# Optimization experiments

Measured on AMD Instinct MI355X. Metric: run time of the kernel, lower is better.

## Reference

```python
import jax, jax.numpy as jnp
import numpy as np

FEAT_STRIDE = 16
PRE_NMS_TOPN = 6000
POST_NMS_TOPN = 300
NMS_THRESH = 0.7
MIN_SIZE = 16.0
NEG = -1e9


def _whctrs(a):
    w = a[2] - a[0] + 1.0
    h = a[3] - a[1] + 1.0
    return w, h, a[0] + 0.5 * (w - 1), a[1] + 0.5 * (h - 1)


def _mkanchors(ws, hs, xc, yc):
    return np.stack([xc - 0.5 * (ws - 1), yc - 0.5 * (hs - 1),
                     xc + 0.5 * (ws - 1), yc + 0.5 * (hs - 1)], axis=1)


def generate_anchors(base_size=16, ratios=(0.5, 1.0, 2.0), scales=(8, 16, 32)):
    base = np.array([0, 0, base_size - 1, base_size - 1], dtype=np.float64)
    w, h, xc, yc = _whctrs(base)
    size = w * h
    ratios = np.array(ratios, dtype=np.float64)
    ws = np.round(np.sqrt(size / ratios))
    hs = np.round(ws * ratios)
    ratio_anchors = _mkanchors(ws, hs, xc, yc)
    out = []
    for a in ratio_anchors:
        w, h, xc, yc = _whctrs(a)
        s = np.array(scales, dtype=np.float64)
        out.append(_mkanchors(w * s, h * s, xc, yc))
    return np.concatenate(out, axis=0).astype(np.float32)


def _nms_single(boxes, scores):
    # boxes [N,4], scores [N] (sorted desc by top_k); greedy NMS, fixed POST_NMS_TOPN picks
    x1, y1, x2, y2 = boxes[:, 0], boxes[:, 1], boxes[:, 2], boxes[:, 3]
    areas = (x2 - x1 + 1.0) * (y2 - y1 + 1.0)

    def body(i, st):
        keep, ok, live = st
        s = jnp.where(live, scores, NEG - 1.0)
        j = jnp.argmax(s)
        valid = s[j] > NEG / 2
        keep = keep.at[i].set(j.astype(jnp.int32))
        ok = ok.at[i].set(valid)
        xx1 = jnp.maximum(x1[j], x1)
        yy1 = jnp.maximum(y1[j], y1)
        xx2 = jnp.minimum(x2[j], x2)
        yy2 = jnp.minimum(y2[j], y2)
        inter = jnp.maximum(xx2 - xx1 + 1.0, 0.0) * jnp.maximum(yy2 - yy1 + 1.0, 0.0)
        iou = inter / (areas[j] + areas - inter)
        live = live & (iou <= NMS_THRESH)
        return keep, ok, live

    keep0 = jnp.zeros((POST_NMS_TOPN,), jnp.int32)
    ok0 = jnp.zeros((POST_NMS_TOPN,), bool)
    live0 = scores > NEG / 2
    keep, ok, _ = jax.lax.fori_loop(0, POST_NMS_TOPN, body, (keep0, ok0, live0))
    return keep, ok


def _proposals(rpn_cls_prob, rpn_bbox_pred, im_info, anchors):
    B, _, H, W = rpn_cls_prob.shape
    A = anchors.shape[0]
    # fg scores: second half of the 2A channel dim
    scores = rpn_cls_prob[:, A:].transpose(0, 2, 3, 1).reshape(B, -1)          # [B, H*W*A]
    deltas = rpn_bbox_pred.transpose(0, 2, 3, 1).reshape(B, -1, 4)             # [B, H*W*A, 4]
    # shifted anchors over the feature map
    sx = (jnp.arange(W, dtype=jnp.float32)) * FEAT_STRIDE
    sy = (jnp.arange(H, dtype=jnp.float32)) * FEAT_STRIDE
    gx, gy = jnp.meshgrid(sx, sy)                                              # [H, W]
    shifts = jnp.stack([gx.ravel(), gy.ravel(), gx.ravel(), gy.ravel()], 1)    # [K, 4]
    all_anchors = (shifts[:, None, :] + anchors[None, :, :]).reshape(-1, 4)    # [K*A, 4]
    # bbox_transform_inv
    wa = all_anchors[:, 2] - all_anchors[:, 0] + 1.0
    ha = all_anchors[:, 3] - all_anchors[:, 1] + 1.0
    cxa = all_anchors[:, 0] + 0.5 * (wa - 1.0)
    cya = all_anchors[:, 1] + 0.5 * (ha - 1.0)
    dx, dy, dw, dh = deltas[..., 0], deltas[..., 1], deltas[..., 2], deltas[..., 3]
    cx = dx * wa + cxa
    cy = dy * ha + cya
    pw = jnp.exp(dw) * wa
    ph = jnp.exp(dh) * ha
    x1 = cx - 0.5 * (pw - 1.0)
    y1 = cy - 0.5 * (ph - 1.0)
    x2 = cx + 0.5 * (pw - 1.0)
    y2 = cy + 0.5 * (ph - 1.0)
    # clip to image
    imh = im_info[:, 0:1]
    imw = im_info[:, 1:2]
    x1 = jnp.clip(x1, 0.0, imw - 1.0)
    y1 = jnp.clip(y1, 0.0, imh - 1.0)
    x2 = jnp.clip(x2, 0.0, imw - 1.0)
    y2 = jnp.clip(y2, 0.0, imh - 1.0)
    boxes = jnp.stack([x1, y1, x2, y2], axis=-1)                               # [B, N, 4]
    # filter boxes smaller than min_size * im_scale (mask by score)
    min_sz = MIN_SIZE * im_info[:, 2:3]
    keep_m = ((x2 - x1 + 1.0) >= min_sz) & ((y2 - y1 + 1.0) >= min_sz)
    scores = jnp.where(keep_m, scores, NEG)
    # pre-NMS top-k
    scores_top, order = jax.lax.top_k(scores, PRE_NMS_TOPN)                    # [B, 6000]
    boxes_top = jnp.take_along_axis(boxes, order[:, :, None], axis=1)          # [B, 6000, 4]
    # greedy NMS per image
    keep, keep_ok = jax.vmap(_nms_single)(boxes_top, scores_top)               # [B, 300]
    sel = jnp.take_along_axis(boxes_top, keep[:, :, None], axis=1)             # [B, 300, 4]
    sel = jnp.where(keep_ok[:, :, None], sel, 0.0)
    bidx = jnp.broadcast_to(jnp.arange(B, dtype=sel.dtype)[:, None, None], (B, POST_NMS_TOPN, 1))
    return jnp.concatenate([bidx, sel], axis=-1)                               # [B, 300, 5]


def setup_inputs() -> dict:
    key = jax.random.key(0)
    k1, k2 = jax.random.split(key)
    B, H, W, A = 32, 100, 100, 9
    rpn_cls_prob = jax.random.uniform(k1, (B, 2 * A, H, W), dtype=jnp.float32)
    rpn_bbox_pred = jax.random.normal(k2, (B, 4 * A, H, W), dtype=jnp.float32) * 0.2
    im_info = jnp.tile(jnp.array([[1600.0, 1600.0, 1.0]], dtype=jnp.float32), (B, 1))
    anchors = jnp.asarray(generate_anchors(base_size=16, ratios=(0.5, 1.0, 2.0), scales=(8, 16, 32)))
    return {"rpn_cls_prob": rpn_cls_prob, "rpn_bbox_pred": rpn_bbox_pred,
            "im_info": im_info, "anchors": anchors}


def reference(rpn_cls_prob, rpn_bbox_pred, im_info, anchors):
    return _proposals(rpn_cls_prob, rpn_bbox_pred, im_info, anchors)
```

## Files before the change

kernel.cpp:

```cpp
#include <hip/hip_runtime.h>

#define NB 32
#define NA 9
#define FH 100
#define FW 100
#define HWSZ (FH*FW)
#define NANCH (HWSZ*NA)
#define PRE 6000
#define POST 300
#define SORTN 8192
#define NEGV -1000000000.0f
#define NMS_T 0.7f
#define MARG 1e-4f
#define NCHUNK ((PRE + 63) / 64)
#define WB() __builtin_amdgcn_wave_barrier()
#define NSLICE 11
#define DSLICE 8192

typedef unsigned long long u64;
typedef unsigned int u32;

__device__ __forceinline__ u32 f2sort(float f) {
  u32 u = __float_as_uint(f);
  return (u & 0x80000000u) ? ~u : (u | 0x80000000u);
}

__device__ __forceinline__ float4 decode_box(const float* __restrict__ pred,
                                             const float* __restrict__ anchors,
                                             int b, int i, float imw, float imh) {
  int hw = i / NA; int a = i - hw * NA;
  int h = hw / FW; int w = hw - h * FW;
  float sx = (float)(w * 16);
  float sy = (float)(h * 16);
  float ax1 = anchors[a*4+0] + sx, ay1 = anchors[a*4+1] + sy;
  float ax2 = anchors[a*4+2] + sx, ay2 = anchors[a*4+3] + sy;
  float wa = ax2 - ax1 + 1.0f, ha = ay2 - ay1 + 1.0f;
  float cxa = ax1 + 0.5f*(wa - 1.0f), cya = ay1 + 0.5f*(ha - 1.0f);
  size_t base = (((size_t)b*36 + a*4)*FH + h)*FW + w;
  float dx = pred[base];
  float dy = pred[base + HWSZ];
  float dw = pred[base + 2*HWSZ];
  float dh = pred[base + 3*HWSZ];
  float cx = dx*wa + cxa, cy = dy*ha + cya;
  float pw = expf(dw)*wa, ph = expf(dh)*ha;
  float x1 = fminf(fmaxf(cx - 0.5f*(pw - 1.0f), 0.0f), imw - 1.0f);
  float y1 = fminf(fmaxf(cy - 0.5f*(ph - 1.0f), 0.0f), imh - 1.0f);
  float x2 = fminf(fmaxf(cx + 0.5f*(pw - 1.0f), 0.0f), imw - 1.0f);
  float y2 = fminf(fmaxf(cy + 0.5f*(ph - 1.0f), 0.0f), imh - 1.0f);
  return make_float4(x1, y1, x2, y2);
}

__global__ void k_zero(u32* __restrict__ histcnt, u32* __restrict__ cand32) {
  int i = blockIdx.x * 1024 + threadIdx.x;
  if (i < 262144) histcnt[i] = 0;
  cand32[i] = 0;
}

__global__ __launch_bounds__(1024) void k_decode(
    const float* __restrict__ cls,
    const float* __restrict__ pred,
    const float* __restrict__ iminfo,
    const float* __restrict__ anchors,
    u32* __restrict__ scoreg,
    u32* __restrict__ histg) {
  __shared__ u32 hl[4096];
  const int blk = blockIdx.x;
  const int b = blk / NSLICE, s = blk - b * NSLICE;
  const int tid = threadIdx.x;
  for (int j = tid; j < 4096; j += 1024) hl[j] = 0;
  __syncthreads();
  const float imh = iminfo[b*3+0], imw = iminfo[b*3+1], sc = iminfo[b*3+2];
  const float msz = 16.0f * sc;
  #pragma unroll
  for (int r = 0; r < 8; ++r) {
    int i = s * DSLICE + r * 1024 + tid;
    if (i < NANCH) {
      int hw = i / NA; int a = i - hw * NA;
      int h = hw / FW; int w = hw - h * FW;
      float score = cls[(((size_t)b*18 + 9 + a)*FH + h)*FW + w];
      float4 bx = decode_box(pred, anchors, b, i, imw, imh);
      bool keep = ((bx.z - bx.x + 1.0f) >= msz) && ((bx.w - bx.y + 1.0f) >= msz);
      float sf = keep ? score : NEGV;
      float t = sf * 4096.0f;
      int bin = (t <= 0.0f) ? 0 : ((t >= 4095.0f) ? 4095 : (int)t);
      atomicAdd(&hl[bin], 1u);
      scoreg[(size_t)b * NANCH + i] = f2sort(sf);
    }
  }
  __syncthreads();
  for (int j = tid; j < 4096; j += 1024) {
    u32 v = hl[j];
    if (v) atomicAdd(&histg[b * 4096 + j], v);
  }
}

__device__ __forceinline__ void w0_cut(u32* hist, u32 target, int lane,
                                       int* cutBin) {
  u32 cs = 0;
  int cb = lane * 64;
  for (int i = 0; i < 64; ++i) cs += hist[cb + ((i + lane) & 63)];
  u32 suf = cs;
  #pragma unroll
  for (int d = 1; d < 64; d <<= 1) {
    u32 o = __shfl_down(suf, (unsigned)d, 64);
    suf += (lane < 64 - d) ? o : 0u;
  }
  u64 m1 = __ballot(suf >= target);
  int L = 63 - __clzll(m1);
  u32 nAb = (L < 63) ? (u32)__builtin_amdgcn_readlane((int)suf, L + 1) : 0u;
  u32 fs = hist[L * 64 + lane];
  #pragma unroll
  for (int d = 1; d < 64; d <<= 1) {
    u32 o = __shfl_down(fs, (unsigned)d, 64);
    fs += (lane < 64 - d) ? o : 0u;
  }
  fs += nAb;
  u64 m2 = __ballot(fs >= target);
  int fb = 63 - __clzll(m2);
  *cutBin = L * 64 + fb;
}

__global__ __launch_bounds__(64) void k_cut(const u32* __restrict__ histg,
                                            u32* __restrict__ thrTg,
                                            u32* __restrict__ binStartG) {
  __shared__ u32 hl[4096];
  const int b = blockIdx.x, lane = threadIdx.x;
  const u32* h = histg + b * 4096;
  for (int i = lane; i < 4096; i += 64) hl[i] = h[i];
  __syncthreads();
  int L;
  w0_cut(hl, PRE, lane, &L);
  u32 running = 0;
  for (int hi = 4095; hi >= L; hi -= 64) {
    int bin = hi - lane;
    u32 c = (bin >= L && bin >= 0) ? hl[bin] : 0u;
    u32 p = c;
    #pragma unroll
    for (int d = 1; d < 64; d <<= 1) {
      u32 o = __shfl_up(p, (unsigned)d, 64);
      if (lane >= d) p += o;
    }
    if (bin >= L && bin >= 0) binStartG[b * 4096 + bin] = running + p - c;
    running += (u32)__builtin_amdgcn_readlane((int)p, 63);
  }
  if (lane == 0) thrTg[b] = f2sort((float)L * (1.0f / 4096.0f));
}

__global__ __launch_bounds__(1024) void k_scatter(
    const u32* __restrict__ scoreg,
    const u32* __restrict__ thrTg,
    const u32* __restrict__ binStartG,
    u32* __restrict__ binCntG,
    u64* __restrict__ candg) {
  const int blk = blockIdx.x;
  const int b = blk / NSLICE, s = blk - b * NSLICE;
  const int tid = threadIdx.x;
  const u32 thrT = thrTg[b];
  const u32* sb = scoreg + (size_t)b * NANCH;
  #pragma unroll
  for (int r = 0; r < 8; ++r) {
    int i = s * DSLICE + r * 1024 + tid;
    if (i < NANCH) {
      u32 sv = sb[i];
      if (sv >= thrT) {
        float f = __uint_as_float(sv ^ 0x80000000u);
        float t = f * 4096.0f;
        int bin = (t >= 4095.0f) ? 4095 : (int)t;
        u32 pos = binStartG[b * 4096 + bin] + atomicAdd(&binCntG[b * 4096 + bin], 1u);
        if (pos < SORTN) candg[(size_t)b * SORTN + pos] = ((u64)sv << 32) | (u32)(~(u32)i);
      }
    }
  }
}

__global__ __launch_bounds__(1024) void k_binsort(
    const u32* __restrict__ binStartG,
    const u32* __restrict__ binCntG,
    u64* __restrict__ candg) {
  __shared__ u64 sc[16][512];
  const int wave = threadIdx.x >> 6, lane = threadIdx.x & 63;
  const int task = blockIdx.x * 16 + wave;
  const int b = task >> 12, bin = task & 4095;
  u32 cnt = binCntG[b * 4096 + bin];
  if (cnt < 2) return;
  u32 base = binStartG[b * 4096 + bin];
  if (base >= SORTN) return;
  u32 m = cnt;
  if (base + m > SORTN) m = SORTN - base;
  u64* seg = candg + (size_t)b * SORTN + base;
  if (m <= 64) {
    u64 v = (lane < (int)m) ? seg[lane] : 0ull;
    #pragma unroll
    for (int k = 2; k <= 64; k <<= 1) {
      for (int j = k >> 1; j > 0; j >>= 1) {
        u64 o = __shfl_xor((unsigned long long)v, j, 64);
        bool dirD = ((lane & k) == 0);
        bool lower = ((lane & j) == 0);
        bool takeMax = (dirD == lower);
        bool sw = takeMax ? (o > v) : (o < v);
        if (sw) v = o;
      }
    }
    if (lane < (int)m) seg[lane] = v;
  } else if (m <= 512) {
    int np = 128; while (np < (int)m) np <<= 1;
    for (int i = lane; i < np; i += 64) sc[wave][i] = (i < (int)m) ? seg[i] : 0ull;
    WB();
    for (int k = 2; k <= np; k <<= 1) {
      for (int j = k >> 1; j > 0; j >>= 1) {
        for (int q = lane; q < np/2; q += 64) {
          int i = ((q & ~(j-1)) << 1) | (q & (j-1));
          int x = i | j;
          u64 a0 = sc[wave][i], a1 = sc[wave][x];
          bool up = (i & k) != 0;
          if (up ? (a0 > a1) : (a0 < a1)) { sc[wave][i] = a1; sc[wave][x] = a0; }
        }
        WB();
      }
    }
    for (int i = lane; i < (int)m; i += 64) seg[i] = sc[wave][i];
  }
}

#define SMEM_BYTES 103424
__global__ __launch_bounds__(1024, 1) void k_nms(
    const u64* __restrict__ candg,
    const float* __restrict__ pred,
    const float* __restrict__ iminfo,
    const float* __restrict__ anchors,
    float* __restrict__ out) {
  __shared__ __align__(16) unsigned char smemRaw[SMEM_BYTES];
  float4* boxes = (float4*)smemRaw;
  u64* liveM = (u64*)(smemRaw + 96256);
  float4* accB = (float4*)(smemRaw + 97024);
  float* accA = (float*)(smemRaw + 101824);
  u64* okm = (u64*)(smemRaw + 103040);
  int* scal = (int*)(smemRaw + 103168);
  float* aL = (float*)(smemRaw + 103232);

  const int b = blockIdx.x;
  const int tid = threadIdx.x;
  const int wave = tid >> 6, lane = tid & 63;
  const u32 liveThr = f2sort(-5.0e8f);
  const u64* cb = candg + (size_t)b * SORTN;

  if (tid < 36) aL[tid] = anchors[tid];
  if (tid == 0) scal[4] = 0;
  __syncthreads();

  const float imh = iminfo[b*3+0], imw = iminfo[b*3+1];
  #pragma unroll
  for (int r = 0; r < 6; ++r) {
    int c = wave + 16 * r;
    if (c < NCHUNK) {
      int i = tid + 1024 * r;
      u64 k = cb[i];
      int idx = (int)(~(u32)k);
      bool v = (u32)idx < (u32)NANCH;
      bool live = ((u32)(k >> 32) > liveThr) && v && (i < PRE);
      int id = v ? idx : 0;
      int hw = id / NA; int a = id - hw * NA;
      int h = hw / FW; int w = hw - h * FW;
      float sx = (float)(w * 16), sy = (float)(h * 16);
      float ax1 = aL[a*4+0] + sx, ay1 = aL[a*4+1] + sy;
      float ax2 = aL[a*4+2] + sx, ay2 = aL[a*4+3] + sy;
      float wa = ax2 - ax1 + 1.0f, ha = ay2 - ay1 + 1.0f;
      float cxa = ax1 + 0.5f*(wa - 1.0f), cya = ay1 + 0.5f*(ha - 1.0f);
      size_t base = (((size_t)b*36 + a*4)*FH + h)*FW + w;
      float dx = pred[base], dy = pred[base + HWSZ];
      float dw = pred[base + 2*HWSZ], dh = pred[base + 3*HWSZ];
      float cx = dx*wa + cxa, cy = dy*ha + cya;
      float pw = expf(dw)*wa, ph = expf(dh)*ha;
      float4 bc;
      bc.x = fminf(fmaxf(cx - 0.5f*(pw - 1.0f), 0.0f), imw - 1.0f);
      bc.y = fminf(fmaxf(cy - 0.5f*(ph - 1.0f), 0.0f), imh - 1.0f);
      bc.z = fminf(fmaxf(cx + 0.5f*(pw - 1.0f), 0.0f), imw - 1.0f);
      bc.w = fminf(fmaxf(cy + 0.5f*(ph - 1.0f), 0.0f), imh - 1.0f);
      boxes[i] = bc;
      u64 lm = __ballot(live);
      if (lane == 0) liveM[c] = lm;
    }
  }
  __syncthreads();

  for (int g = 0; g < NCHUNK; ++g) {
    int nA = scal[4];
    if (nA >= POST) break;
    u64 lm = liveM[g];
    if (lm == 0ull) continue;
    float4 bc = boxes[g * 64 + lane];
    float areaC = (bc.z - bc.x + 1.0f) * (bc.w - bc.y + 1.0f);
    bool ok = (lm >> lane) & 1ull;
    for (int tt = wave; tt < nA; tt += 16) {
      float4 ba = accB[tt];
      float aA = accA[tt];
      float xx1 = fmaxf(ba.x, bc.x);
      float yy1 = fmaxf(ba.y, bc.y);
      float xx2 = fminf(ba.z, bc.z);
      float yy2 = fminf(ba.w, bc.w);
      float inter = fmaxf(xx2 - xx1 + 1.0f, 0.0f) * fmaxf(yy2 - yy1 + 1.0f, 0.0f);
      float un = aA + areaC - inter;
      float q = inter * __builtin_amdgcn_rcpf(un);
      bool hi = q > NMS_T + MARG;
      bool lo = q < NMS_T - MARG;
      bool sup = hi;
      if (__ballot(ok && !hi && !lo)) {
        if (!hi && !lo) sup = (inter / un) > NMS_T;
      }
      ok = ok && !sup;
    }
    u64 wm = __ballot(ok);
    if (lane == 0) okm[wave] = wm;
    __syncthreads();
    if (wave == 0) {
      u64 m = okm[0];
      #pragma unroll
      for (int w = 1; w < 16; ++w) m &= okm[w];
      bool ok0 = (m >> lane) & 1ull;
      int nAcc = nA;
      u64 bal = __ballot(ok0);
      while (bal != 0ull && nAcc < POST) {
        int fl = __ffsll(bal) - 1;
        float ax1 = __int_as_float(__builtin_amdgcn_readlane(__float_as_int(bc.x), fl));
        float ay1 = __int_as_float(__builtin_amdgcn_readlane(__float_as_int(bc.y), fl));
        float ax2 = __int_as_float(__builtin_amdgcn_readlane(__float_as_int(bc.z), fl));
        float ay2 = __int_as_float(__builtin_amdgcn_readlane(__float_as_int(bc.w), fl));
        float aA = (ax2 - ax1 + 1.0f) * (ay2 - ay1 + 1.0f);
        if (lane == 0) { accB[nAcc] = make_float4(ax1, ay1, ax2, ay2); accA[nAcc] = aA; }
        ++nAcc;
        if (ok0) {
          if (lane == fl) ok0 = false;
          else if (lane > fl) {
            float xx1 = fmaxf(ax1, bc.x);
            float yy1 = fmaxf(ay1, bc.y);
            float xx2 = fminf(ax2, bc.z);
            float yy2 = fminf(ay2, bc.w);
            float inter = fmaxf(xx2 - xx1 + 1.0f, 0.0f) * fmaxf(yy2 - yy1 + 1.0f, 0.0f);
            float iou = inter / (aA + areaC - inter);
            if (iou > NMS_T) ok0 = false;
          }
        }
        bal = __ballot(ok0);
      }
      if (lane == 0) scal[4] = nAcc;
    }
    __syncthreads();
  }

  const int nAcc = scal[4];
  float* ob = out + (size_t)b * POST * 5;
  for (int i = tid; i < POST * 5; i += 1024) {
    int row = i / 5, col = i - row * 5;
    float v = 0.f;
    if (col == 0) v = (float)b;
    else if (row < nAcc) {
      float4 bb = accB[row];
      v = (col == 1) ? bb.x : (col == 2) ? bb.y : (col == 3) ? bb.z : bb.w;
    }
    ob[i] = v;
  }
}

extern "C" void kernel_launch(void* const* d_in, const int* in_sizes, int n_in,
                              void* d_out, int out_size, void* d_ws, size_t ws_size,
                              hipStream_t stream) {
  const float* cls     = (const float*)d_in[0];
  const float* pred    = (const float*)d_in[1];
  const float* iminfo  = (const float*)d_in[2];
  const float* anchors = (const float*)d_in[3];
  float* out = (float*)d_out;

  char* ws = (char*)d_ws;
  u32* histg     = (u32*)(ws + 0);
  u32* binCntG   = (u32*)(ws + 524288);
  u32* binStartG = (u32*)(ws + 1048576);
  u32* thrTg     = (u32*)(ws + 1572864);
  u64* candg     = (u64*)(ws + 1572992);
  u32* scoreg    = (u32*)(ws + 3670144);

  k_zero<<<1024, 1024, 0, stream>>>(histg, (u32*)candg);
  k_decode<<<NB*NSLICE, 1024, 0, stream>>>(cls, pred, iminfo, anchors, scoreg, histg);
  k_cut<<<NB, 64, 0, stream>>>(histg, thrTg, binStartG);
  k_scatter<<<NB*NSLICE, 1024, 0, stream>>>(scoreg, thrTg, binStartG, binCntG, candg);
  k_binsort<<<8192, 1024, 0, stream>>>(binStartG, binCntG, candg);
  k_nms<<<NB, 1024, 0, stream>>>(candg, pred, iminfo, anchors, out);
}
```

Baseline: 206.3 us.

## Decode boxes in scatter, carry them through binsort, slim NMS kernel

Decode and scatter now walk anchors in planar (anchor-major) order, so reads of cls and pred are contiguous. Box decoding for surviving candidates moves out of the serial per-image NMS kernel into the parallel scatter kernel, and binsort permutes the boxes along with their keys. NMS becomes a 512-thread block that derives the live mask from a candidate count and lets every wave run the greedy acceptance loop redundantly, removing one barrier per chunk. The cost is extra float4 traffic in scatter and binsort, and candidate zeroing is dropped, which relies on the count to mask stale entries.

After: 213.5 us. 3.5% more time.

```diff
diff --git a/kernel.cpp b/kernel.cpp
--- a/kernel.cpp
+++ b/kernel.cpp
@@ -25,10 +25,10 @@
   return (u & 0x80000000u) ? ~u : (u | 0x80000000u);
 }
 
-__device__ __forceinline__ float4 decode_box(const float* __restrict__ pred,
-                                             const float* __restrict__ anchors,
-                                             int b, int i, float imw, float imh) {
-  int hw = i / NA; int a = i - hw * NA;
+__device__ __forceinline__ float4 decode_box_pm(const float* __restrict__ pred,
+                                                const float* __restrict__ anchors,
+                                                int b, int a, int hw,
+                                                float imw, float imh) {
   int h = hw / FW; int w = hw - h * FW;
   float sx = (float)(w * 16);
   float sy = (float)(h * 16);
@@ -36,7 +36,7 @@
   float ax2 = anchors[a*4+2] + sx, ay2 = anchors[a*4+3] + sy;
   float wa = ax2 - ax1 + 1.0f, ha = ay2 - ay1 + 1.0f;
   float cxa = ax1 + 0.5f*(wa - 1.0f), cya = ay1 + 0.5f*(ha - 1.0f);
-  size_t base = (((size_t)b*36 + a*4)*FH + h)*FW + w;
+  size_t base = ((size_t)b*36 + a*4)*HWSZ + hw;
   float dx = pred[base];
   float dy = pred[base + HWSZ];
   float dw = pred[base + 2*HWSZ];
@@ -50,10 +50,9 @@
   return make_float4(x1, y1, x2, y2);
 }
 
-__global__ void k_zero(u32* __restrict__ histcnt, u32* __restrict__ cand32) {
+__global__ void k_zero(u32* __restrict__ histcnt) {
   int i = blockIdx.x * 1024 + threadIdx.x;
-  if (i < 262144) histcnt[i] = 0;
-  cand32[i] = 0;
+  histcnt[i] = 0;
 }
 
 __global__ __launch_bounds__(1024) void k_decode(
@@ -73,18 +72,17 @@
   const float msz = 16.0f * sc;
   #pragma unroll
   for (int r = 0; r < 8; ++r) {
-    int i = s * DSLICE + r * 1024 + tid;
-    if (i < NANCH) {
-      int hw = i / NA; int a = i - hw * NA;
-      int h = hw / FW; int w = hw - h * FW;
-      float score = cls[(((size_t)b*18 + 9 + a)*FH + h)*FW + w];
-      float4 bx = decode_box(pred, anchors, b, i, imw, imh);
+    int j = s * DSLICE + r * 1024 + tid;
+    if (j < NANCH) {
+      int a = j / HWSZ; int hw = j - a * HWSZ;
+      float score = cls[((size_t)b*18 + 9 + a)*HWSZ + hw];
+      float4 bx = decode_box_pm(pred, anchors, b, a, hw, imw, imh);
       bool keep = ((bx.z - bx.x + 1.0f) >= msz) && ((bx.w - bx.y + 1.0f) >= msz);
       float sf = keep ? score : NEGV;
       float t = sf * 4096.0f;
       int bin = (t <= 0.0f) ? 0 : ((t >= 4095.0f) ? 4095 : (int)t);
       atomicAdd(&hl[bin], 1u);
-      scoreg[(size_t)b * NANCH + i] = f2sort(sf);
+      scoreg[(size_t)b * NANCH + j] = f2sort(sf);
     }
   }
   __syncthreads();
@@ -122,7 +120,8 @@
 
 __global__ __launch_bounds__(64) void k_cut(const u32* __restrict__ histg,
                                             u32* __restrict__ thrTg,
-                                            u32* __restrict__ binStartG) {
+                                            u32* __restrict__ binStartG,
+                                            u32* __restrict__ countG) {
   __shared__ u32 hl[4096];
   const int b = blockIdx.x, lane = threadIdx.x;
   const u32* h = histg + b * 4096;
@@ -143,7 +142,10 @@
     if (bin >= L && bin >= 0) binStartG[b * 4096 + bin] = running + p - c;
     running += (u32)__builtin_amdgcn_readlane((int)p, 63);
   }
-  if (lane == 0) thrTg[b] = f2sort((float)L * (1.0f / 4096.0f));
+  if (lane == 0) {
+    thrTg[b] = f2sort((float)L * (1.0f / 4096.0f));
+    countG[b] = running;
+  }
 }
 
 __global__ __launch_bounds__(1024) void k_scatter(
@@ -151,35 +153,48 @@
     const u32* __restrict__ thrTg,
     const u32* __restrict__ binStartG,
     u32* __restrict__ binCntG,
-    u64* __restrict__ candg) {
+    u64* __restrict__ candg,
+    float4* __restrict__ boxg,
+    const float* __restrict__ pred,
+    const float* __restrict__ iminfo,
+    const float* __restrict__ anchors) {
   const int blk = blockIdx.x;
   const int b = blk / NSLICE, s = blk - b * NSLICE;
   const int tid = threadIdx.x;
   const u32 thrT = thrTg[b];
+  const float imh = iminfo[b*3+0], imw = iminfo[b*3+1];
   const u32* sb = scoreg + (size_t)b * NANCH;
   #pragma unroll
   for (int r = 0; r < 8; ++r) {
-    int i = s * DSLICE + r * 1024 + tid;
-    if (i < NANCH) {
-      u32 sv = sb[i];
+    int j = s * DSLICE + r * 1024 + tid;
+    if (j < NANCH) {
+      u32 sv = sb[j];
       if (sv >= thrT) {
+        int a = j / HWSZ; int hw = j - a * HWSZ;
+        int i = hw * NA + a;
         float f = __uint_as_float(sv ^ 0x80000000u);
         float t = f * 4096.0f;
         int bin = (t >= 4095.0f) ? 4095 : (int)t;
         u32 pos = binStartG[b * 4096 + bin] + atomicAdd(&binCntG[b * 4096 + bin], 1u);
-        if (pos < SORTN) candg[(size_t)b * SORTN + pos] = ((u64)sv << 32) | (u32)(~(u32)i);
-      }
-    }
-  }
-}
-
-__global__ __launch_bounds__(1024) void k_binsort(
+        if (pos < SORTN) {
+          candg[(size_t)b * SORTN + pos] = ((u64)sv << 32) | (u32)(~(u32)i);
+          boxg[(size_t)b * SORTN + pos] = decode_box_pm(pred, anchors, b, a, hw, imw, imh);
+        }
+      }
+    }
+  }
+}
+
+__global__ __launch_bounds__(512) void k_binsort(
     const u32* __restrict__ binStartG,
     const u32* __restrict__ binCntG,
-    u64* __restrict__ candg) {
-  __shared__ u64 sc[16][512];
+    u64* __restrict__ candg,
+    float4* __restrict__ boxg) {
+  __shared__ u64 ks[8][512];
+  __shared__ u32 ops[8][512];
+  __shared__ float4 bs[8][512];
   const int wave = threadIdx.x >> 6, lane = threadIdx.x & 63;
-  const int task = blockIdx.x * 16 + wave;
+  const int task = blockIdx.x * 8 + wave;
   const int b = task >> 12, bin = task & 4095;
   u32 cnt = binCntG[b * 4096 + bin];
   if (cnt < 2) return;
@@ -188,110 +203,84 @@
   u32 m = cnt;
   if (base + m > SORTN) m = SORTN - base;
   u64* seg = candg + (size_t)b * SORTN + base;
+  float4* bseg = boxg + (size_t)b * SORTN + base;
   if (m <= 64) {
     u64 v = (lane < (int)m) ? seg[lane] : 0ull;
+    u32 op = (u32)lane;
     #pragma unroll
     for (int k = 2; k <= 64; k <<= 1) {
       for (int j = k >> 1; j > 0; j >>= 1) {
         u64 o = __shfl_xor((unsigned long long)v, j, 64);
+        u32 oop = __shfl_xor(op, j, 64);
         bool dirD = ((lane & k) == 0);
         bool lower = ((lane & j) == 0);
         bool takeMax = (dirD == lower);
         bool sw = takeMax ? (o > v) : (o < v);
-        if (sw) v = o;
+        if (sw) { v = o; op = oop; }
       }
     }
     if (lane < (int)m) seg[lane] = v;
+    if (lane < (int)m) {
+      float4 bx = bseg[op];
+      bseg[lane] = bx;
+    }
   } else if (m <= 512) {
     int np = 128; while (np < (int)m) np <<= 1;
-    for (int i = lane; i < np; i += 64) sc[wave][i] = (i < (int)m) ? seg[i] : 0ull;
+    for (int i = lane; i < np; i += 64) {
+      ks[wave][i] = (i < (int)m) ? seg[i] : 0ull;
+      ops[wave][i] = (u32)i;
+    }
     WB();
     for (int k = 2; k <= np; k <<= 1) {
       for (int j = k >> 1; j > 0; j >>= 1) {
         for (int q = lane; q < np/2; q += 64) {
           int i = ((q & ~(j-1)) << 1) | (q & (j-1));
           int x = i | j;
-          u64 a0 = sc[wave][i], a1 = sc[wave][x];
+          u64 a0 = ks[wave][i], a1 = ks[wave][x];
           bool up = (i & k) != 0;
-          if (up ? (a0 > a1) : (a0 < a1)) { sc[wave][i] = a1; sc[wave][x] = a0; }
+          if (up ? (a0 > a1) : (a0 < a1)) {
+            ks[wave][i] = a1; ks[wave][x] = a0;
+            u32 t = ops[wave][i]; ops[wave][i] = ops[wave][x]; ops[wave][x] = t;
+          }
         }
         WB();
       }
     }
-    for (int i = lane; i < (int)m; i += 64) seg[i] = sc[wave][i];
-  }
-}
-
-#define SMEM_BYTES 103424
-__global__ __launch_bounds__(1024, 1) void k_nms(
-    const u64* __restrict__ candg,
-    const float* __restrict__ pred,
-    const float* __restrict__ iminfo,
-    const float* __restrict__ anchors,
+    for (int i = lane; i < (int)m; i += 64) bs[wave][i] = bseg[ops[wave][i]];
+    WB();
+    for (int i = lane; i < (int)m; i += 64) {
+      seg[i] = ks[wave][i];
+      bseg[i] = bs[wave][i];
+    }
+  }
+}
+
+__global__ __launch_bounds__(512, 1) void k_nms(
+    const float4* __restrict__ boxg,
+    const u32* __restrict__ countG,
     float* __restrict__ out) {
-  __shared__ __align__(16) unsigned char smemRaw[SMEM_BYTES];
-  float4* boxes = (float4*)smemRaw;
-  u64* liveM = (u64*)(smemRaw + 96256);
-  float4* accB = (float4*)(smemRaw + 97024);
-  float* accA = (float*)(smemRaw + 101824);
-  u64* okm = (u64*)(smemRaw + 103040);
-  int* scal = (int*)(smemRaw + 103168);
-  float* aL = (float*)(smemRaw + 103232);
-
+  __shared__ float4 boxes[NCHUNK * 64];
+  __shared__ float4 accB[POST];
+  __shared__ float accA[POST];
+  __shared__ u64 okm[2][8];
   const int b = blockIdx.x;
   const int tid = threadIdx.x;
   const int wave = tid >> 6, lane = tid & 63;
-  const u32 liveThr = f2sort(-5.0e8f);
-  const u64* cb = candg + (size_t)b * SORTN;
-
-  if (tid < 36) aL[tid] = anchors[tid];
-  if (tid == 0) scal[4] = 0;
+  int cnt = (int)countG[b]; if (cnt > PRE) cnt = PRE;
+  const float4* bg = boxg + (size_t)b * SORTN;
+  for (int i = tid; i < NCHUNK * 64; i += 512) boxes[i] = bg[i];
   __syncthreads();
 
-  const float imh = iminfo[b*3+0], imw = iminfo[b*3+1];
-  #pragma unroll
-  for (int r = 0; r < 6; ++r) {
-    int c = wave + 16 * r;
-    if (c < NCHUNK) {
-      int i = tid + 1024 * r;
-      u64 k = cb[i];
-      int idx = (int)(~(u32)k);
-      bool v = (u32)idx < (u32)NANCH;
-      bool live = ((u32)(k >> 32) > liveThr) && v && (i < PRE);
-      int id = v ? idx : 0;
-      int hw = id / NA; int a = id - hw * NA;
-      int h = hw / FW; int w = hw - h * FW;
-      float sx = (float)(w * 16), sy = (float)(h * 16);
-      float ax1 = aL[a*4+0] + sx, ay1 = aL[a*4+1] + sy;
-      float ax2 = aL[a*4+2] + sx, ay2 = aL[a*4+3] + sy;
-      float wa = ax2 - ax1 + 1.0f, ha = ay2 - ay1 + 1.0f;
-      float cxa = ax1 + 0.5f*(wa - 1.0f), cya = ay1 + 0.5f*(ha - 1.0f);
-      size_t base = (((size_t)b*36 + a*4)*FH + h)*FW + w;
-      float dx = pred[base], dy = pred[base + HWSZ];
-      float dw = pred[base + 2*HWSZ], dh = pred[base + 3*HWSZ];
-      float cx = dx*wa + cxa, cy = dy*ha + cya;
-      float pw = expf(dw)*wa, ph = expf(dh)*ha;
-      float4 bc;
-      bc.x = fminf(fmaxf(cx - 0.5f*(pw - 1.0f), 0.0f), imw - 1.0f);
-      bc.y = fminf(fmaxf(cy - 0.5f*(ph - 1.0f), 0.0f), imh - 1.0f);
-      bc.z = fminf(fmaxf(cx + 0.5f*(pw - 1.0f), 0.0f), imw - 1.0f);
-      bc.w = fminf(fmaxf(cy + 0.5f*(ph - 1.0f), 0.0f), imh - 1.0f);
-      boxes[i] = bc;
-      u64 lm = __ballot(live);
-      if (lane == 0) liveM[c] = lm;
-    }
-  }
-  __syncthreads();
-
+  int nAcc = 0, lc = 0;
   for (int g = 0; g < NCHUNK; ++g) {
-    int nA = scal[4];
-    if (nA >= POST) break;
-    u64 lm = liveM[g];
-    if (lm == 0ull) continue;
+    if (nAcc >= POST) break;
+    int nliv = cnt - g * 64;
+    if (nliv <= 0) break;
+    u64 lm = (nliv >= 64) ? ~0ull : ((1ull << nliv) - 1ull);
     float4 bc = boxes[g * 64 + lane];
     float areaC = (bc.z - bc.x + 1.0f) * (bc.w - bc.y + 1.0f);
     bool ok = (lm >> lane) & 1ull;
-    for (int tt = wave; tt < nA; tt += 16) {
+    for (int tt = wave; tt < nAcc; tt += 8) {
       float4 ba = accB[tt];
       float aA = accA[tt];
       float xx1 = fmaxf(ba.x, bc.x);
@@ -310,46 +299,41 @@
       ok = ok && !sup;
     }
     u64 wm = __ballot(ok);
-    if (lane == 0) okm[wave] = wm;
+    if (lane == 0) okm[lc & 1][wave] = wm;
     __syncthreads();
-    if (wave == 0) {
-      u64 m = okm[0];
-      #pragma unroll
-      for (int w = 1; w < 16; ++w) m &= okm[w];
-      bool ok0 = (m >> lane) & 1ull;
-      int nAcc = nA;
-      u64 bal = __ballot(ok0);
-      while (bal != 0ull && nAcc < POST) {
-        int fl = __ffsll(bal) - 1;
-        float ax1 = __int_as_float(__builtin_amdgcn_readlane(__float_as_int(bc.x), fl));
-        float ay1 = __int_as_float(__builtin_amdgcn_readlane(__float_as_int(bc.y), fl));
-        float ax2 = __int_as_float(__builtin_amdgcn_readlane(__float_as_int(bc.z), fl));
-        float ay2 = __int_as_float(__builtin_amdgcn_readlane(__float_as_int(bc.w), fl));
-        float aA = (ax2 - ax1 + 1.0f) * (ay2 - ay1 + 1.0f);
-        if (lane == 0) { accB[nAcc] = make_float4(ax1, ay1, ax2, ay2); accA[nAcc] = aA; }
-        ++nAcc;
-        if (ok0) {
-          if (lane == fl) ok0 = false;
-          else if (lane > fl) {
-            float xx1 = fmaxf(ax1, bc.x);
-            float yy1 = fmaxf(ay1, bc.y);
-            float xx2 = fminf(ax2, bc.z);
-            float yy2 = fminf(ay2, bc.w);
-            float inter = fmaxf(xx2 - xx1 + 1.0f, 0.0f) * fmaxf(yy2 - yy1 + 1.0f, 0.0f);
-            float iou = inter / (aA + areaC - inter);
-            if (iou > NMS_T) ok0 = false;
-          }
+    u64 mm = okm[lc & 1][0];
+    #pragma unroll
+    for (int w = 1; w < 8; ++w) mm &= okm[lc & 1][w];
+    ++lc;
+    bool ok0 = (mm >> lane) & 1ull;
+    u64 bal = __ballot(ok0);
+    while (bal != 0ull && nAcc < POST) {
+      int fl = __ffsll(bal) - 1;
+      float ax1 = __int_as_float(__builtin_amdgcn_readlane(__float_as_int(bc.x), fl));
+      float ay1 = __int_as_float(__builtin_amdgcn_readlane(__float_as_int(bc.y), fl));
+      float ax2 = __int_as_float(__builtin_amdgcn_readlane(__float_as_int(bc.z), fl));
+      float ay2 = __int_as_float(__builtin_amdgcn_readlane(__float_as_int(bc.w), fl));
+      float aA = (ax2 - ax1 + 1.0f) * (ay2 - ay1 + 1.0f);
+      if (lane == 0) { accB[nAcc] = make_float4(ax1, ay1, ax2, ay2); accA[nAcc] = aA; }
+      ++nAcc;
+      if (ok0) {
+        if (lane == fl) ok0 = false;
+        else if (lane > fl) {
+          float xx1 = fmaxf(ax1, bc.x);
+          float yy1 = fmaxf(ay1, bc.y);
+          float xx2 = fminf(ax2, bc.z);
+          float yy2 = fminf(ay2, bc.w);
+          float inter = fmaxf(xx2 - xx1 + 1.0f, 0.0f) * fmaxf(yy2 - yy1 + 1.0f, 0.0f);
+          float iou = inter / (aA + areaC - inter);
+          if (iou > NMS_T) ok0 = false;
         }
-        bal = __ballot(ok0);
-      }
-      if (lane == 0) scal[4] = nAcc;
-    }
-    __syncthreads();
-  }
-
-  const int nAcc = scal[4];
+      }
+      bal = __ballot(ok0);
+    }
+  }
+
   float* ob = out + (size_t)b * POST * 5;
-  for (int i = tid; i < POST * 5; i += 1024) {
+  for (int i = tid; i < POST * 5; i += 512) {
     int row = i / 5, col = i - row * 5;
     float v = 0.f;
     if (col == 0) v = (float)b;
@@ -375,13 +359,16 @@
   u32* binCntG   = (u32*)(ws + 524288);
   u32* binStartG = (u32*)(ws + 1048576);
   u32* thrTg     = (u32*)(ws + 1572864);
-  u64* candg     = (u64*)(ws + 1572992);
-  u32* scoreg    = (u32*)(ws + 3670144);
-
-  k_zero<<<1024, 1024, 0, stream>>>(histg, (u32*)candg);
+  u32* countG    = (u32*)(ws + 1572992);
+  u64* candg     = (u64*)(ws + 1573120);
+  float4* boxg   = (float4*)(ws + 3670272);
+  u32* scoreg    = (u32*)(ws + 7864576);
+
+  k_zero<<<256, 1024, 0, stream>>>(histg);
   k_decode<<<NB*NSLICE, 1024, 0, stream>>>(cls, pred, iminfo, anchors, scoreg, histg);
-  k_cut<<<NB, 64, 0, stream>>>(histg, thrTg, binStartG);
-  k_scatter<<<NB*NSLICE, 1024, 0, stream>>>(scoreg, thrTg, binStartG, binCntG, candg);
-  k_binsort<<<8192, 1024, 0, stream>>>(binStartG, binCntG, candg);
-  k_nms<<<NB, 1024, 0, stream>>>(candg, pred, iminfo, anchors, out);
-}
+  k_cut<<<NB, 64, 0, stream>>>(histg, thrTg, binStartG, countG);
+  k_scatter<<<NB*NSLICE, 1024, 0, stream>>>(scoreg, thrTg, binStartG, binCntG,
+                                            candg, boxg, pred, iminfo, anchors);
+  k_binsort<<<16384, 512, 0, stream>>>(binStartG, binCntG, candg, boxg);
+  k_nms<<<NB, 512, 0, stream>>>(boxg, countG, out);
+}
```
